# Optimization experiments

Hardware: AMD Instinct MI355X
Metric: run time of the kernel (lower is better)

The kernel has to match this reference:

```python
import jax, jax.numpy as jnp
import numpy as np

N, F_IN, UNITS, HEADS = 4096, 128, 64, 4
EDGE_P = 0.01  # adjacency density


def setup_inputs() -> dict:
    key = jax.random.key(0)
    k1, k2, k3, k4, k5 = jax.random.split(key, 5)
    inputs = jax.random.normal(k1, (N, F_IN), dtype=jnp.float32)
    adj = jax.random.bernoulli(k2, EDGE_P, (N, N)).astype(jnp.float32)
    # glorot-normal-ish parameter scales
    w = jax.random.normal(k3, (F_IN, UNITS), dtype=jnp.float32) * np.float32(np.sqrt(2.0 / (F_IN + UNITS)))
    attn_w1 = jax.random.normal(k4, (UNITS, HEADS), dtype=jnp.float32) * np.float32(np.sqrt(2.0 / (UNITS + HEADS)))
    attn_w2 = jax.random.normal(k5, (UNITS, HEADS), dtype=jnp.float32) * np.float32(np.sqrt(2.0 / (UNITS + HEADS)))
    return {"inputs": inputs, "adj": adj, "w": w, "attn_w1": attn_w1, "attn_w2": attn_w2}


def reference(inputs, adj, w, attn_w1, attn_w2):
    # dropout=0, bias=0, final_layer=False, activation=relu
    x = inputs @ w                                  # [N, U]
    e1 = x @ attn_w1                                # [N, H]
    e2 = x @ attn_w2                                # [N, H]
    # coeffs[i, j, h] = relu(e1[i, h] + e2[j, h])
    coeffs = jax.nn.relu(e1[:, None, :] + e2[None, :, :])   # [N, N, H]
    # NOTE: original multiplies by adj (zeros -> logit 0, not -inf) then softmax over j
    scores = adj[:, :, None] * coeffs               # [N, N, H]
    attn = jax.nn.softmax(scores, axis=1)           # normalize over neighbors j
    # per-head aggregation, concat heads -> [N, H*U] (head-major blocks)
    out = jnp.einsum("ijh,ju->ihu", attn, x).reshape(N, HEADS * UNITS)
    return jax.nn.relu(out)
```

## Files before the change

kernel.cpp:

```cpp
#include <hip/hip_runtime.h>
#include <hip/hip_bf16.h>

#define N_NODES 4096
#define F_IN    128
#define UNITS   64
#define HEADS   4

__global__ __launch_bounds__(256) void k1(const float* __restrict__ inputs,
                                          const float* __restrict__ w,
                                          const float* __restrict__ aw1,
                                          const float* __restrict__ aw2,
                                          float* __restrict__ x,
                                          float* __restrict__ e1,
                                          float* __restrict__ e2,
                                          float* __restrict__ partial) {
    __shared__ float w_lds[F_IN * UNITS];
    __shared__ float in_lds[16 * F_IN];
    __shared__ float x_lds[16 * 65];

    const int t = threadIdx.x;
    const int b = blockIdx.x;
    const int row0 = b * 16;

    for (int k = t; k < F_IN * UNITS; k += 256) w_lds[k] = w[k];
    for (int k = t; k < 16 * F_IN; k += 256) in_lds[k] = inputs[(size_t)row0 * F_IN + k];
    __syncthreads();

    const int u = t & 63;
    const int rg = t >> 6;
    for (int s = 0; s < 4; s++) {
        const int r = rg * 4 + s;
        float acc = 0.f;
#pragma unroll 8
        for (int k = 0; k < F_IN; k++)
            acc = fmaf(in_lds[r * F_IN + k], w_lds[k * UNITS + u], acc);
        x_lds[r * 65 + u] = acc;
        x[(size_t)(row0 + r) * UNITS + u] = acc;
    }
    __syncthreads();

    if (t < 128) {
        const int r = t >> 3;
        const int rem = t & 7;
        const int h = rem & 3;
        const bool first = rem < 4;
        const float* aw = first ? aw1 : aw2;
        float s = 0.f;
#pragma unroll 8
        for (int uu = 0; uu < UNITS; uu++)
            s += x_lds[r * 65 + uu] * aw[uu * HEADS + h];
        (first ? e1 : e2)[(size_t)(row0 + r) * HEADS + h] = s;
    }

    if (t < 64) {
        float s = 0.f;
#pragma unroll
        for (int r = 0; r < 16; r++) s += x_lds[r * 65 + t];
        partial[b * 64 + t] = s;
    }
}

__global__ __launch_bounds__(64) void k1b(const float* __restrict__ partial,
                                          float* __restrict__ S) {
    const int t = threadIdx.x;
    float s = 0.f;
    for (int b = 0; b < 256; b++) s += partial[b * 64 + t];
    S[t] = s;
}

__global__ __launch_bounds__(256) void k2(const float* __restrict__ adj,
                                          const float* __restrict__ x,
                                          const float* __restrict__ e1,
                                          const float* __restrict__ e2,
                                          const float* __restrict__ S,
                                          float* __restrict__ out) {
    __shared__ unsigned short nbr[N_NODES];
    __shared__ int cnt;

    const int i = blockIdx.x;
    const int t = threadIdx.x;

    if (t == 0) cnt = 0;
    __syncthreads();

    const float4* arow = (const float4*)(adj + (size_t)i * N_NODES);
#pragma unroll
    for (int it = 0; it < 4; it++) {
        const int c = t + it * 256;
        const float4 v = arow[c];
        const int base = c * 4;
        if (v.x != 0.f) nbr[atomicAdd(&cnt, 1)] = (unsigned short)(base + 0);
        if (v.y != 0.f) nbr[atomicAdd(&cnt, 1)] = (unsigned short)(base + 1);
        if (v.z != 0.f) nbr[atomicAdd(&cnt, 1)] = (unsigned short)(base + 2);
        if (v.w != 0.f) nbr[atomicAdd(&cnt, 1)] = (unsigned short)(base + 3);
    }
    __syncthreads();

    const int n = cnt;
    const int h = t >> 6;
    const int u = t & 63;
    const float e1h = e1[(size_t)i * HEADS + h];

    float acc = 0.f;
    float den = 0.f;
#pragma unroll 2
    for (int k = 0; k < n; k++) {
        const int j = nbr[k];
        const float sc = fmaxf(e1h + e2[j * HEADS + h], 0.f);
        const float wgt = __expf(sc) - 1.f;
        den += wgt;
        acc = fmaf(wgt, x[j * UNITS + u], acc);
    }

    const float numer = S[u] + acc;
    const float denom = (float)N_NODES + den;
    out[(size_t)i * (HEADS * UNITS) + t] = fmaxf(numer / denom, 0.f);
}

extern "C" void kernel_launch(void* const* d_in, const int* in_sizes, int n_in,
                              void* d_out, int out_size, void* d_ws, size_t ws_size,
                              hipStream_t stream) {
    const float* inputs = (const float*)d_in[0];
    const float* adj    = (const float*)d_in[1];
    const float* w      = (const float*)d_in[2];
    const float* aw1    = (const float*)d_in[3];
    const float* aw2    = (const float*)d_in[4];
    float* out = (float*)d_out;

    float* ws = (float*)d_ws;
    float* x       = ws;
    float* e1      = ws + 262144;
    float* e2      = ws + 262144 + 16384;
    float* partial = ws + 262144 + 2 * 16384;
    float* S       = ws + 262144 + 3 * 16384;

    k1<<<256, 256, 0, stream>>>(inputs, w, aw1, aw2, x, e1, e2, partial);
    k1b<<<1, 64, 0, stream>>>(partial, S);
    k2<<<N_NODES, 256, 0, stream>>>(adj, x, e1, e2, S, out);
}
```

Baseline: 133.1 us.

## Vectorize k1 matmul with transposed weights, parallelize k1b, precompute attention weights in k2

k1 now stores the weight matrix transposed with a padded pitch and computes four rows per thread with float4 LDS reads, loading the inputs with float4 copies. k1b splits the 256-block reduction across four wavefronts and combines them in shared memory. k2 computes the exp weights for all four heads once per neighbor chunk into shared memory, instead of every thread recomputing them, at the cost of two barriers per chunk. The dominant cost is probably k2's 64 MB adjacency read, so the gains may be small.

```diff
diff --git a/kernel.cpp b/kernel.cpp
--- a/kernel.cpp
+++ b/kernel.cpp
@@ -5,6 +5,8 @@
 #define F_IN    128
 #define UNITS   64
 #define HEADS   4
+#define WT_PITCH 132
+#define CHUNK   128
 
 __global__ __launch_bounds__(256) void k1(const float* __restrict__ inputs,
                                           const float* __restrict__ w,
@@ -14,7 +16,7 @@
                                           float* __restrict__ e1,
                                           float* __restrict__ e2,
                                           float* __restrict__ partial) {
-    __shared__ float w_lds[F_IN * UNITS];
+    __shared__ float w_t[UNITS * WT_PITCH];
     __shared__ float in_lds[16 * F_IN];
     __shared__ float x_lds[16 * 65];
 
@@ -22,21 +24,43 @@
     const int b = blockIdx.x;
     const int row0 = b * 16;
 
-    for (int k = t; k < F_IN * UNITS; k += 256) w_lds[k] = w[k];
-    for (int k = t; k < 16 * F_IN; k += 256) in_lds[k] = inputs[(size_t)row0 * F_IN + k];
+    for (int idx = t; idx < F_IN * UNITS; idx += 256) {
+        const int u = idx & 63;
+        const int k = idx >> 6;
+        w_t[u * WT_PITCH + k] = w[idx];
+    }
+    {
+        const float4* src = (const float4*)(inputs + (size_t)row0 * F_IN);
+        float4* dst = (float4*)in_lds;
+        for (int idx = t; idx < 16 * F_IN / 4; idx += 256) dst[idx] = src[idx];
+    }
     __syncthreads();
 
     const int u = t & 63;
     const int rg = t >> 6;
-    for (int s = 0; s < 4; s++) {
-        const int r = rg * 4 + s;
-        float acc = 0.f;
+    float acc0 = 0.f, acc1 = 0.f, acc2 = 0.f, acc3 = 0.f;
+    const float4* wrow = (const float4*)(w_t + u * WT_PITCH);
+    const float4* i0 = (const float4*)(in_lds + (rg * 4 + 0) * F_IN);
+    const float4* i1 = (const float4*)(in_lds + (rg * 4 + 1) * F_IN);
+    const float4* i2 = (const float4*)(in_lds + (rg * 4 + 2) * F_IN);
+    const float4* i3 = (const float4*)(in_lds + (rg * 4 + 3) * F_IN);
 #pragma unroll 8
-        for (int k = 0; k < F_IN; k++)
-            acc = fmaf(in_lds[r * F_IN + k], w_lds[k * UNITS + u], acc);
-        x_lds[r * 65 + u] = acc;
-        x[(size_t)(row0 + r) * UNITS + u] = acc;
+    for (int c = 0; c < F_IN / 4; c++) {
+        const float4 wv = wrow[c];
+        float4 v;
+        v = i0[c]; acc0 = fmaf(wv.x, v.x, fmaf(wv.y, v.y, fmaf(wv.z, v.z, fmaf(wv.w, v.w, acc0))));
+        v = i1[c]; acc1 = fmaf(wv.x, v.x, fmaf(wv.y, v.y, fmaf(wv.z, v.z, fmaf(wv.w, v.w, acc1))));
+        v = i2[c]; acc2 = fmaf(wv.x, v.x, fmaf(wv.y, v.y, fmaf(wv.z, v.z, fmaf(wv.w, v.w, acc2))));
+        v = i3[c]; acc3 = fmaf(wv.x, v.x, fmaf(wv.y, v.y, fmaf(wv.z, v.z, fmaf(wv.w, v.w, acc3))));
     }
+    x_lds[(rg * 4 + 0) * 65 + u] = acc0;
+    x_lds[(rg * 4 + 1) * 65 + u] = acc1;
+    x_lds[(rg * 4 + 2) * 65 + u] = acc2;
+    x_lds[(rg * 4 + 3) * 65 + u] = acc3;
+    x[(size_t)(row0 + rg * 4 + 0) * UNITS + u] = acc0;
+    x[(size_t)(row0 + rg * 4 + 1) * UNITS + u] = acc1;
+    x[(size_t)(row0 + rg * 4 + 2) * UNITS + u] = acc2;
+    x[(size_t)(row0 + rg * 4 + 3) * UNITS + u] = acc3;
     __syncthreads();
 
     if (t < 128) {
@@ -60,12 +84,17 @@
     }
 }
 
-__global__ __launch_bounds__(64) void k1b(const float* __restrict__ partial,
-                                          float* __restrict__ S) {
-    const int t = threadIdx.x;
+__global__ __launch_bounds__(256) void k1b(const float* __restrict__ partial,
+                                           float* __restrict__ S) {
+    __shared__ float red[4][64];
+    const int u = threadIdx.x & 63;
+    const int q = threadIdx.x >> 6;
     float s = 0.f;
-    for (int b = 0; b < 256; b++) s += partial[b * 64 + t];
-    S[t] = s;
+#pragma unroll 8
+    for (int b = q; b < 256; b += 4) s += partial[b * 64 + u];
+    red[q][u] = s;
+    __syncthreads();
+    if (threadIdx.x < 64) S[u] = red[0][u] + red[1][u] + red[2][u] + red[3][u];
 }
 
 __global__ __launch_bounds__(256) void k2(const float* __restrict__ adj,
@@ -75,6 +104,7 @@
                                           const float* __restrict__ S,
                                           float* __restrict__ out) {
     __shared__ unsigned short nbr[N_NODES];
+    __shared__ float wgt[CHUNK * 4];
     __shared__ int cnt;
 
     const int i = blockIdx.x;
@@ -99,17 +129,35 @@
     const int n = cnt;
     const int h = t >> 6;
     const int u = t & 63;
-    const float e1h = e1[(size_t)i * HEADS + h];
+
+    const float4 e1v = *(const float4*)(e1 + (size_t)i * HEADS);
 
     float acc = 0.f;
     float den = 0.f;
-#pragma unroll 2
-    for (int k = 0; k < n; k++) {
-        const int j = nbr[k];
-        const float sc = fmaxf(e1h + e2[j * HEADS + h], 0.f);
-        const float wgt = __expf(sc) - 1.f;
-        den += wgt;
-        acc = fmaf(wgt, x[j * UNITS + u], acc);
+
+    for (int base = 0; base < n; base += CHUNK) {
+        const int m = min(n - base, CHUNK);
+
+        if (t < m) {
+            const int j = nbr[base + t];
+            const float4 e2v = *(const float4*)(e2 + (size_t)j * HEADS);
+            float4 wv;
+            wv.x = __expf(fmaxf(e1v.x + e2v.x, 0.f)) - 1.f;
+            wv.y = __expf(fmaxf(e1v.y + e2v.y, 0.f)) - 1.f;
+            wv.z = __expf(fmaxf(e1v.z + e2v.z, 0.f)) - 1.f;
+            wv.w = __expf(fmaxf(e1v.w + e2v.w, 0.f)) - 1.f;
+            *(float4*)(wgt + t * 4) = wv;
+        }
+        __syncthreads();
+
+#pragma unroll 4
+        for (int k = 0; k < m; k++) {
+            const int j = nbr[base + k];
+            const float wv = wgt[k * 4 + h];
+            den += wv;
+            acc = fmaf(wv, x[j * UNITS + u], acc);
+        }
+        __syncthreads();
     }
 
     const float numer = S[u] + acc;
@@ -135,6 +183,6 @@
     float* S       = ws + 262144 + 3 * 16384;
 
     k1<<<256, 256, 0, stream>>>(inputs, w, aw1, aw2, x, e1, e2, partial);
-    k1b<<<1, 64, 0, stream>>>(partial, S);
+    k1b<<<1, 256, 0, stream>>>(partial, S);
     k2<<<N_NODES, 256, 0, stream>>>(adj, x, e1, e2, S, out);
 }
```

Measured after the change: 121.1 us. 9.0% less time.
